# Optimization experiments

Measured on AMD Instinct MI355X. Metric: run time of the kernel, lower is better.

## Reference

```python
import jax, jax.numpy as jnp
import numpy as np

N_NODES = 100000
N_EDGES = 1600000
D = 64
ED = 16
N_LAYERS = 3
NEG_SLOPE = 0.2


def gat_conv(x, src, dst, ea, W, a_src, a_dst, W_e, a_e, b):
    """Single-head PyG GATConv with edge_dim, self-loops already appended."""
    N = x.shape[0]
    h = x @ W                                   # [N, D]
    s_src = h @ a_src                           # [N]
    s_dst = h @ a_dst                           # [N]
    s_edge = (ea @ W_e) @ a_e                   # [Etot]
    alpha = s_src[src] + s_dst[dst] + s_edge    # [Etot]
    alpha = jnp.where(alpha >= 0, alpha, NEG_SLOPE * alpha)  # leaky_relu(0.2)
    # segment softmax over destination node
    m = jax.ops.segment_max(alpha, dst, num_segments=N)
    e = jnp.exp(alpha - m[dst])
    z = jax.ops.segment_sum(e, dst, num_segments=N)
    w = e / z[dst]                              # [Etot]
    out = jax.ops.segment_sum(w[:, None] * h[src], dst, num_segments=N)
    return out + b


def setup_inputs() -> dict:
    key = jax.random.key(0)
    ks = jax.random.split(key, 8)
    sc = 1.0 / np.sqrt(D)
    return {
        "x": jax.random.normal(ks[0], (N_NODES, D), jnp.float32),
        "edge_index": jax.random.randint(ks[1], (2, N_EDGES), 0, N_NODES, jnp.int32),
        "edge_attr": jax.random.normal(ks[2], (N_EDGES, ED), jnp.float32),
        "Ws": jax.random.normal(ks[3], (N_LAYERS, D, D), jnp.float32) * sc,
        "att_srcs": jax.random.normal(ks[4], (N_LAYERS, D), jnp.float32) * sc,
        "att_dsts": jax.random.normal(ks[5], (N_LAYERS, D), jnp.float32) * sc,
        "W_edges": jax.random.normal(ks[6], (N_LAYERS, ED, D), jnp.float32) * sc,
        "att_edges": jax.random.normal(ks[7], (N_LAYERS, D), jnp.float32) * sc,
        "biases": jnp.zeros((N_LAYERS, D), jnp.float32),
        "batch_size": 100,
    }


def reference(x, edge_index, edge_attr, Ws, att_srcs, att_dsts, W_edges, att_edges, biases, batch_size):
    N = x.shape[0]
    # add self loops (PyG fill_value='mean' for self-loop edge_attr)
    loops = jnp.arange(N, dtype=edge_index.dtype)
    src = jnp.concatenate([edge_index[0], loops])
    dst = jnp.concatenate([edge_index[1], loops])
    ea = jnp.concatenate(
        [edge_attr, jnp.broadcast_to(edge_attr.mean(0), (N, edge_attr.shape[1]))], axis=0
    )
    for l in range(N_LAYERS):
        x = gat_conv(x, src, dst, ea, Ws[l], att_srcs[l], att_dsts[l],
                     W_edges[l], att_edges[l], biases[l])
        x = jax.nn.gelu(x, approximate=False)  # torch F.gelu default = exact
        # dropout is identity in eval mode
    return x.reshape(batch_size, N // batch_size, D)
```

## Files before the change

kernel.cpp:

```cpp
#include <hip/hip_runtime.h>
#include <math.h>

#define NN 100000
#define NE 1600000
#define ET (NN + NE)
#define D 64
#define EDIM 16

static __device__ __forceinline__ float leaky(float a) { return a >= 0.f ? a : 0.2f * a; }

__global__ __launch_bounds__(256) void k_init(int* __restrict__ deg, float* __restrict__ meansum,
                                              float* __restrict__ w16, const float* __restrict__ We,
                                              const float* __restrict__ ae) {
    int i = blockIdx.x * 256 + threadIdx.x;
    if (i < NN) deg[i] = 1;
    if (blockIdx.x == 0) {
        int t = threadIdx.x;
        if (t < 16) meansum[t] = 0.f;
        if (t < 48) {
            int l = t >> 4, k = t & 15;
            const float* wr = We + l * (EDIM * D) + k * D;
            const float* av = ae + l * D;
            float s = 0.f;
#pragma unroll
            for (int j = 0; j < D; j++) s += wr[j] * av[j];
            w16[t] = s;
        }
    }
}

__global__ __launch_bounds__(256) void k_edge(const int* __restrict__ ei, const float* __restrict__ ea,
                                              const float* __restrict__ w16, int* __restrict__ deg,
                                              float* __restrict__ sedge3, float* __restrict__ meansum) {
    int tid = blockIdx.x * blockDim.x + threadIdx.x;
    int stride = gridDim.x * blockDim.x;
    float wr[48];
#pragma unroll
    for (int c = 0; c < 48; c++) wr[c] = w16[c];
    float ms[16];
#pragma unroll
    for (int c = 0; c < 16; c++) ms[c] = 0.f;
    for (int e = tid; e < NE; e += stride) {
        int d = ei[NE + e];
        atomicAdd(&deg[d], 1);
        const float4* ea4 = (const float4*)(ea + (size_t)e * EDIM);
        float4 v0 = ea4[0], v1 = ea4[1], v2 = ea4[2], v3 = ea4[3];
        float vv[16] = {v0.x, v0.y, v0.z, v0.w, v1.x, v1.y, v1.z, v1.w,
                        v2.x, v2.y, v2.z, v2.w, v3.x, v3.y, v3.z, v3.w};
#pragma unroll
        for (int c = 0; c < 16; c++) ms[c] += vv[c];
#pragma unroll
        for (int l = 0; l < 3; l++) {
            float s = 0.f;
#pragma unroll
            for (int c = 0; c < 16; c++) s += vv[c] * wr[l * 16 + c];
            sedge3[(size_t)l * NE + e] = s;
        }
    }
#pragma unroll
    for (int c = 0; c < 16; c++)
        for (int o = 32; o; o >>= 1) ms[c] += __shfl_xor(ms[c], o);
    __shared__ float bsum[16];
    if (threadIdx.x < 16) bsum[threadIdx.x] = 0.f;
    __syncthreads();
    if ((threadIdx.x & 63) == 0)
        for (int c = 0; c < 16; c++) atomicAdd(&bsum[c], ms[c]);
    __syncthreads();
    if (threadIdx.x < 16) atomicAdd(&meansum[threadIdx.x], bsum[threadIdx.x]);
}

__global__ __launch_bounds__(256) void k_scan1(const int* __restrict__ deg, int* __restrict__ rowstart,
                                               int* __restrict__ blocksum) {
    __shared__ int sd[256];
    int t = threadIdx.x;
    int i = blockIdx.x * 256 + t;
    int v = (i < NN) ? deg[i] : 0;
    sd[t] = v;
    __syncthreads();
    for (int o = 1; o < 256; o <<= 1) {
        int x = sd[t];
        int y = (t >= o) ? sd[t - o] : 0;
        __syncthreads();
        sd[t] = x + y;
        __syncthreads();
    }
    int incl = sd[t];
    if (i < NN) rowstart[i] = incl - v;
    if (t == 255) blocksum[blockIdx.x] = incl;
}

__global__ __launch_bounds__(512) void k_scan2(const int* __restrict__ blocksum, int* __restrict__ blockoff,
                                               int* __restrict__ rowstart, const float* __restrict__ meansum,
                                               const float* __restrict__ w16, float* __restrict__ slw, int nb) {
    __shared__ int sd[512];
    int t = threadIdx.x;
    int v = (t < nb) ? blocksum[t] : 0;
    sd[t] = v;
    __syncthreads();
    for (int o = 1; o < 512; o <<= 1) {
        int x = sd[t];
        int y = (t >= o) ? sd[t - o] : 0;
        __syncthreads();
        sd[t] = x + y;
        __syncthreads();
    }
    if (t < nb) blockoff[t] = sd[t] - v;
    if (t == 0) rowstart[NN] = ET;
    if (t < 3) {
        float s = 0.f;
        for (int k = 0; k < 16; k++) s += (meansum[k] * (1.0f / NE)) * w16[t * 16 + k];
        slw[t] = s;
    }
}

__global__ __launch_bounds__(256) void k_scan3(int* __restrict__ rowstart, const int* __restrict__ blockoff,
                                               int* __restrict__ cursor) {
    int i = blockIdx.x * 256 + threadIdx.x;
    if (i < NN) {
        int r = rowstart[i] + blockoff[i >> 8];
        rowstart[i] = r;
        cursor[i] = r;
    }
}

__global__ __launch_bounds__(256) void k_scatter(const int* __restrict__ ei, const float* __restrict__ sedge3,
                                                 const float* __restrict__ slw, int* __restrict__ cursor,
                                                 float4* __restrict__ csr) {
    int tid = blockIdx.x * blockDim.x + threadIdx.x;
    int stride = gridDim.x * blockDim.x;
    float s0 = slw[0], s1 = slw[1], s2 = slw[2];
    for (int e = tid; e < ET; e += stride) {
        int s, d;
        float a0, a1, a2;
        if (e < NE) {
            s = ei[e];
            d = ei[NE + e];
            a0 = sedge3[e];
            a1 = sedge3[(size_t)NE + e];
            a2 = sedge3[2 * (size_t)NE + e];
        } else {
            s = d = e - NE;
            a0 = s0; a1 = s1; a2 = s2;
        }
        int pos = atomicAdd(&cursor[d], 1);
        csr[pos] = make_float4(__int_as_float(s), a0, a1, a2);
    }
}

__global__ __launch_bounds__(256) void k_gemm(const float* __restrict__ x, const float* __restrict__ W,
                                              const float* __restrict__ asrc, const float* __restrict__ adst,
                                              float* __restrict__ h, float* __restrict__ ssrc,
                                              float* __restrict__ sdst) {
    int t = threadIdx.x;
    int lane = t & 63;
    int wv = __builtin_amdgcn_readfirstlane(t >> 6);
    int row0 = blockIdx.x * 64 + wv * 16;
    float Wreg[64];
#pragma unroll
    for (int k = 0; k < 64; k++) Wreg[k] = W[k * 64 + lane];
    float asl = asrc[lane], adl = adst[lane];
    for (int rr = 0; rr < 16; rr++) {
        int r = row0 + rr;
        if (r >= NN) break;
        const float* xr = x + (size_t)r * 64;
        float acc = 0.f;
#pragma unroll
        for (int k = 0; k < 64; k++) acc = fmaf(xr[k], Wreg[k], acc);
        h[(size_t)r * 64 + lane] = acc;
        float ps = acc * asl, pd = acc * adl;
#pragma unroll
        for (int o = 32; o; o >>= 1) {
            ps += __shfl_xor(ps, o);
            pd += __shfl_xor(pd, o);
        }
        if (lane == 0) {
            ssrc[r] = ps;
            sdst[r] = pd;
        }
    }
}

template <int LAYER>
__global__ __launch_bounds__(256) void k_agg(const float4* __restrict__ csr, const int* __restrict__ rowstart,
                                             const float* __restrict__ ssrc, const float* __restrict__ sdst,
                                             const float* __restrict__ h, const float* __restrict__ bias,
                                             float* __restrict__ out) {
    int t = threadIdx.x;
    int lane = t & 63;
    int wv = __builtin_amdgcn_readfirstlane(t >> 6);
    int n = blockIdx.x * 4 + wv;
    int start = rowstart[n];
    int dg = rowstart[n + 1] - start;
    float sd = sdst[n];
    float m = -1e30f;
    for (int i = lane; i < dg; i += 64) {
        float4 rec = csr[start + i];
        float se = (LAYER == 0) ? rec.y : ((LAYER == 1) ? rec.z : rec.w);
        int s = __float_as_int(rec.x);
        m = fmaxf(m, leaky(ssrc[s] + sd + se));
    }
#pragma unroll
    for (int o = 32; o; o >>= 1) m = fmaxf(m, __shfl_xor(m, o));
    float acc = 0.f, z = 0.f;
    for (int base = 0; base < dg; base += 64) {
        int i = base + lane;
        float ew = 0.f;
        int es = 0;
        if (i < dg) {
            float4 rec = csr[start + i];
            float se = (LAYER == 0) ? rec.y : ((LAYER == 1) ? rec.z : rec.w);
            es = __float_as_int(rec.x);
            ew = __expf(leaky(ssrc[es] + sd + se) - m);
        }
        z += ew;
        int cnt = min(64, dg - base);
        for (int j = 0; j < cnt; j++) {
            float wj = __shfl(ew, j);
            int sj = __shfl(es, j);
            acc = fmaf(wj, h[(size_t)sj * 64 + lane], acc);
        }
    }
#pragma unroll
    for (int o = 32; o; o >>= 1) z += __shfl_xor(z, o);
    float v = acc / z + bias[lane];
    float g = 0.5f * v * (1.0f + erff(v * 0.70710678118654752f));
    out[(size_t)n * 64 + lane] = g;
}

extern "C" void kernel_launch(void* const* d_in, const int* in_sizes, int n_in,
                              void* d_out, int out_size, void* d_ws, size_t ws_size,
                              hipStream_t stream) {
    const float* x0 = (const float*)d_in[0];
    const int* ei = (const int*)d_in[1];
    const float* ea = (const float*)d_in[2];
    const float* Ws = (const float*)d_in[3];
    const float* asrc = (const float*)d_in[4];
    const float* adst = (const float*)d_in[5];
    const float* We = (const float*)d_in[6];
    const float* ae = (const float*)d_in[7];
    const float* bias = (const float*)d_in[8];

    char* wsb = (char*)d_ws;
    size_t off = 0;
    auto alloc = [&](size_t bytes) -> char* {
        char* p = wsb + off;
        off += (bytes + 255) & ~(size_t)255;
        return p;
    };
    float* xA = (float*)alloc((size_t)NN * D * 4);
    float* xB = (float*)alloc((size_t)NN * D * 4);
    float* h = (float*)alloc((size_t)NN * D * 4);
    float* ssrc = (float*)alloc((size_t)NN * 4);
    float* sdst = (float*)alloc((size_t)NN * 4);
    float* sedge3 = (float*)alloc(3 * (size_t)NE * 4);
    float4* csr = (float4*)alloc((size_t)ET * 16);
    int* deg = (int*)alloc((size_t)NN * 4);
    int* rowstart = (int*)alloc((size_t)(NN + 1) * 4);
    int* cursor = (int*)alloc((size_t)NN * 4);
    int* blocksum = (int*)alloc(512 * 4);
    int* blockoff = (int*)alloc(512 * 4);
    float* meansum = (float*)alloc(16 * 4);
    float* w16 = (float*)alloc(48 * 4);
    float* slw = (float*)alloc(3 * 4);

    int nb = (NN + 255) / 256;
    k_init<<<nb, 256, 0, stream>>>(deg, meansum, w16, We, ae);
    k_edge<<<1024, 256, 0, stream>>>(ei, ea, w16, deg, sedge3, meansum);
    k_scan1<<<nb, 256, 0, stream>>>(deg, rowstart, blocksum);
    k_scan2<<<1, 512, 0, stream>>>(blocksum, blockoff, rowstart, meansum, w16, slw, nb);
    k_scan3<<<nb, 256, 0, stream>>>(rowstart, blockoff, cursor);
    k_scatter<<<2048, 256, 0, stream>>>(ei, sedge3, slw, cursor, csr);

    float* outp = (float*)d_out;
    int gg = (NN + 63) / 64;
    k_gemm<<<gg, 256, 0, stream>>>(x0, Ws, asrc, adst, h, ssrc, sdst);
    k_agg<0><<<NN / 4, 256, 0, stream>>>(csr, rowstart, ssrc, sdst, h, bias, xA);
    k_gemm<<<gg, 256, 0, stream>>>(xA, Ws + 4096, asrc + 64, adst + 64, h, ssrc, sdst);
    k_agg<1><<<NN / 4, 256, 0, stream>>>(csr, rowstart, ssrc, sdst, h, bias + 64, xB);
    k_gemm<<<gg, 256, 0, stream>>>(xB, Ws + 8192, asrc + 128, adst + 128, h, ssrc, sdst);
    k_agg<2><<<NN / 4, 256, 0, stream>>>(csr, rowstart, ssrc, sdst, h, bias + 128, outp);
}
```

Measured before the change: 839.0 us.

## Use global upper-bound softmax shift and precomputed edge ranks for CSR build

Replaces the per-destination max pass in each aggregation with a bound built from global maxima of source and edge scores, tracked via ordered-uint atomicMax. This removes one full gather pass over CSR records and source scores per layer. The CSR scatter now uses ranks captured from the degree-count atomics instead of a second atomic cursor pass, and full 64-edge chunks get an unrolled inner loop. It risks exp underflow if score spreads are large, and it stores ranks as 16-bit values.

```diff
diff --git a/kernel.cpp b/kernel.cpp
--- a/kernel.cpp
+++ b/kernel.cpp
@@ -9,7 +9,17 @@
 
 static __device__ __forceinline__ float leaky(float a) { return a >= 0.f ? a : 0.2f * a; }
 
+static __device__ __forceinline__ unsigned fmap(float f) {
+    unsigned u = __float_as_uint(f);
+    return (u & 0x80000000u) ? ~u : (u | 0x80000000u);
+}
+static __device__ __forceinline__ float funmap(unsigned u) {
+    unsigned f = (u & 0x80000000u) ? (u ^ 0x80000000u) : ~u;
+    return __uint_as_float(f);
+}
+
 __global__ __launch_bounds__(256) void k_init(int* __restrict__ deg, float* __restrict__ meansum,
+                                              unsigned* __restrict__ gse_u, unsigned* __restrict__ gsrc_u,
                                               float* __restrict__ w16, const float* __restrict__ We,
                                               const float* __restrict__ ae) {
     int i = blockIdx.x * 256 + threadIdx.x;
@@ -17,6 +27,10 @@
     if (blockIdx.x == 0) {
         int t = threadIdx.x;
         if (t < 16) meansum[t] = 0.f;
+        if (t < 3) {
+            gse_u[t] = fmap(-3.0e38f);
+            gsrc_u[t] = fmap(-3.0e38f);
+        }
         if (t < 48) {
             int l = t >> 4, k = t & 15;
             const float* wr = We + l * (EDIM * D) + k * D;
@@ -31,7 +45,9 @@
 
 __global__ __launch_bounds__(256) void k_edge(const int* __restrict__ ei, const float* __restrict__ ea,
                                               const float* __restrict__ w16, int* __restrict__ deg,
-                                              float* __restrict__ sedge3, float* __restrict__ meansum) {
+                                              unsigned short* __restrict__ rank16,
+                                              float* __restrict__ sedge3, float* __restrict__ meansum,
+                                              unsigned* __restrict__ gse_u) {
     int tid = blockIdx.x * blockDim.x + threadIdx.x;
     int stride = gridDim.x * blockDim.x;
     float wr[48];
@@ -40,9 +56,11 @@
     float ms[16];
 #pragma unroll
     for (int c = 0; c < 16; c++) ms[c] = 0.f;
+    float smax[3] = {-3e38f, -3e38f, -3e38f};
     for (int e = tid; e < NE; e += stride) {
         int d = ei[NE + e];
-        atomicAdd(&deg[d], 1);
+        int rank = atomicAdd(&deg[d], 1);
+        rank16[e] = (unsigned short)rank;
         const float4* ea4 = (const float4*)(ea + (size_t)e * EDIM);
         float4 v0 = ea4[0], v1 = ea4[1], v2 = ea4[2], v3 = ea4[3];
         float vv[16] = {v0.x, v0.y, v0.z, v0.w, v1.x, v1.y, v1.z, v1.w,
@@ -55,18 +73,27 @@
 #pragma unroll
             for (int c = 0; c < 16; c++) s += vv[c] * wr[l * 16 + c];
             sedge3[(size_t)l * NE + e] = s;
+            smax[l] = fmaxf(smax[l], s);
         }
     }
 #pragma unroll
     for (int c = 0; c < 16; c++)
         for (int o = 32; o; o >>= 1) ms[c] += __shfl_xor(ms[c], o);
+#pragma unroll
+    for (int l = 0; l < 3; l++)
+        for (int o = 32; o; o >>= 1) smax[l] = fmaxf(smax[l], __shfl_xor(smax[l], o));
     __shared__ float bsum[16];
+    __shared__ unsigned bmax[3];
     if (threadIdx.x < 16) bsum[threadIdx.x] = 0.f;
+    if (threadIdx.x < 3) bmax[threadIdx.x] = fmap(-3e38f);
     __syncthreads();
-    if ((threadIdx.x & 63) == 0)
+    if ((threadIdx.x & 63) == 0) {
         for (int c = 0; c < 16; c++) atomicAdd(&bsum[c], ms[c]);
+        for (int l = 0; l < 3; l++) atomicMax(&bmax[l], fmap(smax[l]));
+    }
     __syncthreads();
     if (threadIdx.x < 16) atomicAdd(&meansum[threadIdx.x], bsum[threadIdx.x]);
+    if (threadIdx.x < 3) atomicMax(&gse_u[threadIdx.x], bmax[threadIdx.x]);
 }
 
 __global__ __launch_bounds__(256) void k_scan1(const int* __restrict__ deg, int* __restrict__ rowstart,
@@ -91,7 +118,9 @@
 
 __global__ __launch_bounds__(512) void k_scan2(const int* __restrict__ blocksum, int* __restrict__ blockoff,
                                                int* __restrict__ rowstart, const float* __restrict__ meansum,
-                                               const float* __restrict__ w16, float* __restrict__ slw, int nb) {
+                                               const float* __restrict__ w16, float* __restrict__ slw,
+                                               const unsigned* __restrict__ gse_u, float* __restrict__ gse_f,
+                                               int nb) {
     __shared__ int sd[512];
     int t = threadIdx.x;
     int v = (t < nb) ? blocksum[t] : 0;
@@ -110,27 +139,24 @@
         float s = 0.f;
         for (int k = 0; k < 16; k++) s += (meansum[k] * (1.0f / NE)) * w16[t * 16 + k];
         slw[t] = s;
-    }
-}
-
-__global__ __launch_bounds__(256) void k_scan3(int* __restrict__ rowstart, const int* __restrict__ blockoff,
-                                               int* __restrict__ cursor) {
+        gse_f[t] = fmaxf(funmap(gse_u[t]), s);
+    }
+}
+
+__global__ __launch_bounds__(256) void k_scan3(int* __restrict__ rowstart, const int* __restrict__ blockoff) {
     int i = blockIdx.x * 256 + threadIdx.x;
-    if (i < NN) {
-        int r = rowstart[i] + blockoff[i >> 8];
-        rowstart[i] = r;
-        cursor[i] = r;
-    }
+    if (i < NN) rowstart[i] = rowstart[i] + blockoff[i >> 8];
 }
 
 __global__ __launch_bounds__(256) void k_scatter(const int* __restrict__ ei, const float* __restrict__ sedge3,
-                                                 const float* __restrict__ slw, int* __restrict__ cursor,
-                                                 float4* __restrict__ csr) {
+                                                 const float* __restrict__ slw,
+                                                 const unsigned short* __restrict__ rank16,
+                                                 const int* __restrict__ rowstart, float4* __restrict__ csr) {
     int tid = blockIdx.x * blockDim.x + threadIdx.x;
     int stride = gridDim.x * blockDim.x;
     float s0 = slw[0], s1 = slw[1], s2 = slw[2];
     for (int e = tid; e < ET; e += stride) {
-        int s, d;
+        int s, d, pos;
         float a0, a1, a2;
         if (e < NE) {
             s = ei[e];
@@ -138,11 +164,12 @@
             a0 = sedge3[e];
             a1 = sedge3[(size_t)NE + e];
             a2 = sedge3[2 * (size_t)NE + e];
+            pos = rowstart[d] + rank16[e];
         } else {
             s = d = e - NE;
             a0 = s0; a1 = s1; a2 = s2;
-        }
-        int pos = atomicAdd(&cursor[d], 1);
+            pos = rowstart[d];
+        }
         csr[pos] = make_float4(__int_as_float(s), a0, a1, a2);
     }
 }
@@ -150,7 +177,7 @@
 __global__ __launch_bounds__(256) void k_gemm(const float* __restrict__ x, const float* __restrict__ W,
                                               const float* __restrict__ asrc, const float* __restrict__ adst,
                                               float* __restrict__ h, float* __restrict__ ssrc,
-                                              float* __restrict__ sdst) {
+                                              float* __restrict__ sdst, unsigned* __restrict__ gsrcu) {
     int t = threadIdx.x;
     int lane = t & 63;
     int wv = __builtin_amdgcn_readfirstlane(t >> 6);
@@ -159,6 +186,7 @@
 #pragma unroll
     for (int k = 0; k < 64; k++) Wreg[k] = W[k * 64 + lane];
     float asl = asrc[lane], adl = adst[lane];
+    float wmax = -3e38f;
     for (int rr = 0; rr < 16; rr++) {
         int r = row0 + rr;
         if (r >= NN) break;
@@ -173,17 +201,20 @@
             ps += __shfl_xor(ps, o);
             pd += __shfl_xor(pd, o);
         }
+        wmax = fmaxf(wmax, ps);
         if (lane == 0) {
             ssrc[r] = ps;
             sdst[r] = pd;
         }
     }
+    if (lane == 0) atomicMax(gsrcu, fmap(wmax));
 }
 
 template <int LAYER>
 __global__ __launch_bounds__(256) void k_agg(const float4* __restrict__ csr, const int* __restrict__ rowstart,
                                              const float* __restrict__ ssrc, const float* __restrict__ sdst,
                                              const float* __restrict__ h, const float* __restrict__ bias,
+                                             const unsigned* __restrict__ gsrcu, const float* __restrict__ gsef,
                                              float* __restrict__ out) {
     int t = threadIdx.x;
     int lane = t & 63;
@@ -192,15 +223,7 @@
     int start = rowstart[n];
     int dg = rowstart[n + 1] - start;
     float sd = sdst[n];
-    float m = -1e30f;
-    for (int i = lane; i < dg; i += 64) {
-        float4 rec = csr[start + i];
-        float se = (LAYER == 0) ? rec.y : ((LAYER == 1) ? rec.z : rec.w);
-        int s = __float_as_int(rec.x);
-        m = fmaxf(m, leaky(ssrc[s] + sd + se));
-    }
-#pragma unroll
-    for (int o = 32; o; o >>= 1) m = fmaxf(m, __shfl_xor(m, o));
+    float M = leaky(funmap(gsrcu[0]) + sd + gsef[LAYER]);
     float acc = 0.f, z = 0.f;
     for (int base = 0; base < dg; base += 64) {
         int i = base + lane;
@@ -210,14 +233,23 @@
             float4 rec = csr[start + i];
             float se = (LAYER == 0) ? rec.y : ((LAYER == 1) ? rec.z : rec.w);
             es = __float_as_int(rec.x);
-            ew = __expf(leaky(ssrc[es] + sd + se) - m);
+            ew = __expf(leaky(ssrc[es] + sd + se) - M);
         }
         z += ew;
         int cnt = min(64, dg - base);
-        for (int j = 0; j < cnt; j++) {
-            float wj = __shfl(ew, j);
-            int sj = __shfl(es, j);
-            acc = fmaf(wj, h[(size_t)sj * 64 + lane], acc);
+        if (cnt == 64) {
+#pragma unroll 4
+            for (int j = 0; j < 64; j++) {
+                float wj = __shfl(ew, j);
+                int sj = __shfl(es, j);
+                acc = fmaf(wj, h[(size_t)sj * 64 + lane], acc);
+            }
+        } else {
+            for (int j = 0; j < cnt; j++) {
+                float wj = __shfl(ew, j);
+                int sj = __shfl(es, j);
+                acc = fmaf(wj, h[(size_t)sj * 64 + lane], acc);
+            }
         }
     }
 #pragma unroll
@@ -254,29 +286,32 @@
     float* sdst = (float*)alloc((size_t)NN * 4);
     float* sedge3 = (float*)alloc(3 * (size_t)NE * 4);
     float4* csr = (float4*)alloc((size_t)ET * 16);
+    unsigned short* rank16 = (unsigned short*)alloc((size_t)NE * 2);
     int* deg = (int*)alloc((size_t)NN * 4);
     int* rowstart = (int*)alloc((size_t)(NN + 1) * 4);
-    int* cursor = (int*)alloc((size_t)NN * 4);
     int* blocksum = (int*)alloc(512 * 4);
     int* blockoff = (int*)alloc(512 * 4);
     float* meansum = (float*)alloc(16 * 4);
     float* w16 = (float*)alloc(48 * 4);
     float* slw = (float*)alloc(3 * 4);
+    unsigned* gse_u = (unsigned*)alloc(3 * 4);
+    float* gse_f = (float*)alloc(3 * 4);
+    unsigned* gsrc_u = (unsigned*)alloc(3 * 4);
 
     int nb = (NN + 255) / 256;
-    k_init<<<nb, 256, 0, stream>>>(deg, meansum, w16, We, ae);
-    k_edge<<<1024, 256, 0, stream>>>(ei, ea, w16, deg, sedge3, meansum);
+    k_init<<<nb, 256, 0, stream>>>(deg, meansum, gse_u, gsrc_u, w16, We, ae);
+    k_edge<<<1024, 256, 0, stream>>>(ei, ea, w16, deg, rank16, sedge3, meansum, gse_u);
     k_scan1<<<nb, 256, 0, stream>>>(deg, rowstart, blocksum);
-    k_scan2<<<1, 512, 0, stream>>>(blocksum, blockoff, rowstart, meansum, w16, slw, nb);
-    k_scan3<<<nb, 256, 0, stream>>>(rowstart, blockoff, cursor);
-    k_scatter<<<2048, 256, 0, stream>>>(ei, sedge3, slw, cursor, csr);
+    k_scan2<<<1, 512, 0, stream>>>(blocksum, blockoff, rowstart, meansum, w16, slw, gse_u, gse_f, nb);
+    k_scan3<<<nb, 256, 0, stream>>>(rowstart, blockoff);
+    k_scatter<<<2048, 256, 0, stream>>>(ei, sedge3, slw, rank16, rowstart, csr);
 
     float* outp = (float*)d_out;
     int gg = (NN + 63) / 64;
-    k_gemm<<<gg, 256, 0, stream>>>(x0, Ws, asrc, adst, h, ssrc, sdst);
-    k_agg<0><<<NN / 4, 256, 0, stream>>>(csr, rowstart, ssrc, sdst, h, bias, xA);
-    k_gemm<<<gg, 256, 0, stream>>>(xA, Ws + 4096, asrc + 64, adst + 64, h, ssrc, sdst);
-    k_agg<1><<<NN / 4, 256, 0, stream>>>(csr, rowstart, ssrc, sdst, h, bias + 64, xB);
-    k_gemm<<<gg, 256, 0, stream>>>(xB, Ws + 8192, asrc + 128, adst + 128, h, ssrc, sdst);
-    k_agg<2><<<NN / 4, 256, 0, stream>>>(csr, rowstart, ssrc, sdst, h, bias + 128, outp);
-}
+    k_gemm<<<gg, 256, 0, stream>>>(x0, Ws, asrc, adst, h, ssrc, sdst, gsrc_u + 0);
+    k_agg<0><<<NN / 4, 256, 0, stream>>>(csr, rowstart, ssrc, sdst, h, bias, gsrc_u + 0, gse_f, xA);
+    k_gemm<<<gg, 256, 0, stream>>>(xA, Ws + 4096, asrc + 64, adst + 64, h, ssrc, sdst, gsrc_u + 1);
+    k_agg<1><<<NN / 4, 256, 0, stream>>>(csr, rowstart, ssrc, sdst, h, bias + 64, gsrc_u + 1, gse_f, xB);
+    k_gemm<<<gg, 256, 0, stream>>>(xB, Ws + 8192, asrc + 128, adst + 128, h, ssrc, sdst, gsrc_u + 2);
+    k_agg<2><<<NN / 4, 256, 0, stream>>>(csr, rowstart, ssrc, sdst, h, bias + 128, gsrc_u + 2, gse_f, outp);
+}
```

After: 910.4 us. +8.5%, slower.
